# Performance work log

Hardware: AMD Instinct MI355X
Metric: run time of the kernel (lower is better)

The kernel has to match this reference:

```python
import jax, jax.numpy as jnp
import numpy as np

N = 50_000      # nodes
E = 800_000     # edges (before self-loops)
D = 128         # in_dim == out_dim
H, C = 4, 32    # GAT heads, per-head channels (out_dim // 4)
NEG_SLOPE = 0.2
LN_EPS = 1e-5


def setup_inputs() -> dict:
    key = jax.random.key(0)
    ks = jax.random.split(key, 8)
    s = 0.05
    return {
        "x": jax.random.normal(ks[0], (N, D), jnp.float32),
        "gat_W": jax.random.normal(ks[1], (D, H * C), jnp.float32) * s,
        "att_src": jax.random.normal(ks[2], (H, C), jnp.float32) * s,
        "att_dst": jax.random.normal(ks[3], (H, C), jnp.float32) * s,
        "gat_bias": jnp.zeros((H * C,), jnp.float32),
        "gcn_W": jax.random.normal(ks[4], (D, D), jnp.float32) * s,
        "gcn_bias": jnp.zeros((D,), jnp.float32),
        "gate_W": jax.random.normal(ks[5], (2 * D, 2), jnp.float32) * s,
        "gate_b": jnp.zeros((2,), jnp.float32),
        "ln_gamma": jnp.ones((D,), jnp.float32),
        "ln_beta": jnp.zeros((D,), jnp.float32),
        "edge_index": jax.random.randint(ks[6], (2, E), 0, N, jnp.int64),
    }


def reference(x, gat_W, att_src, att_dst, gat_bias, gcn_W, gcn_bias,
              gate_W, gate_b, ln_gamma, ln_beta, edge_index):
    n = x.shape[0]
    # PyG default: add self-loops for both GATConv and GCNConv
    loops = jnp.arange(n, dtype=edge_index.dtype)
    src = jnp.concatenate([edge_index[0], loops])  # message source j
    dst = jnp.concatenate([edge_index[1], loops])  # aggregation target i

    # ---------------- GATConv (heads=4, concat=True) ----------------
    h = (x @ gat_W).reshape(n, H, C)               # [N,H,C]
    a_src = jnp.einsum('nhc,hc->nh', h, att_src)   # [N,H]
    a_dst = jnp.einsum('nhc,hc->nh', h, att_dst)
    e = a_src[src] + a_dst[dst]                    # [Et,H]
    e = jnp.where(e > 0, e, NEG_SLOPE * e)         # LeakyReLU(0.2)
    e_max = jax.ops.segment_max(e, dst, num_segments=n)   # scatter-softmax, stable
    w = jnp.exp(e - e_max[dst])
    w_sum = jax.ops.segment_sum(w, dst, num_segments=n)
    alpha = w / w_sum[dst]                         # [Et,H]
    msg = alpha[:, :, None] * h[src]               # [Et,H,C]
    gat_out = jax.ops.segment_sum(msg, dst, num_segments=n).reshape(n, H * C) + gat_bias

    # ---------------- GCNConv (sym-normalized, self-loops) ----------------
    deg = jax.ops.segment_sum(jnp.ones_like(dst, dtype=x.dtype), dst, num_segments=n)
    dinv = jnp.where(deg > 0, deg ** -0.5, 0.0)
    norm = dinv[src] * dinv[dst]                   # [Et]
    g = x @ gcn_W                                  # [N,D]
    gcn_out = jax.ops.segment_sum(norm[:, None] * g[src], dst, num_segments=n) + gcn_bias

    # ---------------- gated fusion + residual + LayerNorm ----------------
    gate = jax.nn.softmax(jnp.concatenate([gat_out, gcn_out], axis=1) @ gate_W + gate_b, axis=-1)
    out = gate[:, 0:1] * gat_out + gate[:, 1:2] * gcn_out
    y = out + x
    mu = y.mean(axis=-1, keepdims=True)
    var = y.var(axis=-1, keepdims=True)
    return (y - mu) * jax.lax.rsqrt(var + LN_EPS) * ln_gamma + ln_beta
```

## Files before the change

### kernel.cpp

```cpp
#include <hip/hip_runtime.h>
#include <math.h>


typedef __attribute__((ext_vector_type(8))) short    bf16x8;
typedef __attribute__((ext_vector_type(4))) float    f32x4;
typedef __attribute__((ext_vector_type(8))) unsigned short u16x8;

__device__ __forceinline__ unsigned short f2bf(float f) {
    unsigned int u = __float_as_uint(f);
    u += 0x7fffu + ((u >> 16) & 1u);
    return (unsigned short)(u >> 16);
}
__device__ __forceinline__ float bfhi(unsigned int u) {
    return __uint_as_float(u & 0xffff0000u);
}
__device__ __forceinline__ float bflo(unsigned int u) {
    return __uint_as_float(u << 16);
}

__global__ __launch_bounds__(256) void k_prep(
    const float* __restrict__ Wg, const float* __restrict__ Wc,
    unsigned short* __restrict__ wt, int* __restrict__ counts, int n)
{
    const int t = blockIdx.x * 256 + threadIdx.x;
    const int nn = t >> 4;
    const int k0 = (t & 15) * 8;
    const float* Wsrc = (nn < 128) ? (Wg + nn) : (Wc + (nn - 128));
    u16x8 u;
    #pragma unroll
    for (int j = 0; j < 8; ++j) u[j] = f2bf(Wsrc[(size_t)(k0 + j) * 128]);
    *reinterpret_cast<u16x8*>(wt + (size_t)t * 8) = u;
    for (int i = t; i < n; i += 4096) counts[i] = 0;
}

__global__ void k_hist(const int* __restrict__ dst, int* __restrict__ counts, int E)
{
    int i = blockIdx.x * blockDim.x + threadIdx.x;
    if (i < E) atomicAdd(&counts[dst[i]], 1);
}

__global__ __launch_bounds__(256) void k_scan1(const int* __restrict__ counts,
                                               int* __restrict__ bsum, int n)
{
    __shared__ int sh[256];
    int t = threadIdx.x;
    int i = blockIdx.x * 256 + t;
    sh[t] = (i < n) ? counts[i] : 0;
    __syncthreads();
    #pragma unroll
    for (int off = 128; off >= 1; off >>= 1) {
        if (t < off) sh[t] += sh[t + off];
        __syncthreads();
    }
    if (t == 0) bsum[blockIdx.x] = sh[0];
}

__global__ __launch_bounds__(256) void k_scan2(int* __restrict__ bsum, int nb)
{
    __shared__ int sh[256];
    int t = threadIdx.x;
    int v = (t < nb) ? bsum[t] : 0;
    sh[t] = v;
    __syncthreads();
    #pragma unroll
    for (int off = 1; off < 256; off <<= 1) {
        int u = (t >= off) ? sh[t - off] : 0;
        __syncthreads();
        sh[t] += u;
        __syncthreads();
    }
    if (t < nb) bsum[t] = sh[t] - v;
}

__global__ __launch_bounds__(256) void k_scan3(
    const int* __restrict__ counts, const int* __restrict__ bsum,
    int* __restrict__ rowptr, int* __restrict__ cursor,
    float* __restrict__ dinv, int n)
{
    __shared__ int sh[256];
    int t = threadIdx.x;
    int i = blockIdx.x * 256 + t;
    int v = (i < n) ? counts[i] : 0;
    sh[t] = v;
    __syncthreads();
    #pragma unroll
    for (int off = 1; off < 256; off <<= 1) {
        int u = (t >= off) ? sh[t - off] : 0;
        __syncthreads();
        sh[t] += u;
        __syncthreads();
    }
    if (i < n) {
        int excl = bsum[blockIdx.x] + sh[t] - v;
        rowptr[i] = excl;
        cursor[i] = excl;
        dinv[i] = rsqrtf((float)(1 + v));
        if (i == n - 1) rowptr[n] = excl + v;
    }
}

__global__ __launch_bounds__(256) void k_combo(
    const float* __restrict__ x, const unsigned short* __restrict__ wt,
    const float* __restrict__ att_src, const float* __restrict__ att_dst,
    const float* __restrict__ dinv, unsigned short* __restrict__ pk,
    float* __restrict__ a_src, float* __restrict__ a_dst, int n)
{
    __shared__ unsigned short wlds[32768];
    const int t = threadIdx.x;

    char* lbase = (char*)wlds;
    #pragma unroll
    for (int i = 0; i < 16; ++i) {
        const int ch = i * 256 + t;
        const int nn = ch >> 4;
        const int off = (ch & 15) * 16;
        const int byte = (nn * 256 + off) ^ ((nn & 7) << 4);
        *reinterpret_cast<u16x8*>(lbase + byte) =
            *reinterpret_cast<const u16x8*>(wt + (size_t)ch * 8);
    }
    __syncthreads();

    const int l = t & 63;
    const int row0 = blockIdx.x * 64 + (t >> 6) * 16;
    const int arow = row0 + (l & 15);
    const bool av = arow < n;
    const float* xp = x + (size_t)arow * 128 + (l >> 4) * 8;

    bf16x8 afr[4];
    #pragma unroll
    for (int ks = 0; ks < 4; ++ks) {
        float4 u0 = av ? *reinterpret_cast<const float4*>(xp + ks * 32)
                       : make_float4(0.f, 0.f, 0.f, 0.f);
        float4 u1 = av ? *reinterpret_cast<const float4*>(xp + ks * 32 + 4)
                       : make_float4(0.f, 0.f, 0.f, 0.f);
        bf16x8 a;
        a[0] = (short)f2bf(u0.x); a[1] = (short)f2bf(u0.y);
        a[2] = (short)f2bf(u0.z); a[3] = (short)f2bf(u0.w);
        a[4] = (short)f2bf(u1.x); a[5] = (short)f2bf(u1.y);
        a[6] = (short)f2bf(u1.z); a[7] = (short)f2bf(u1.w);
        afr[ks] = a;
    }

    f32x4 acc[16];
    #pragma unroll
    for (int ni = 0; ni < 16; ++ni) acc[ni] = (f32x4){0.f, 0.f, 0.f, 0.f};

    const int bco = (l & 15) * 256 + (l >> 4) * 16;
    const int bxo = (l & 7) << 4;
    #pragma unroll
    for (int ks = 0; ks < 4; ++ks) {
        #pragma unroll
        for (int ni = 0; ni < 16; ++ni) {
            const int byte = ((ni * 16) * 256 + bco + ks * 64) ^ bxo;
            const bf16x8 b = *reinterpret_cast<const bf16x8*>(lbase + byte);
            acc[ni] = __builtin_amdgcn_mfma_f32_16x16x32_bf16(afr[ks], b, acc[ni], 0, 0, 0);
        }
    }

    float ps[4][4], pd[4][4];
    #pragma unroll
    for (int h = 0; h < 4; ++h)
        #pragma unroll
        for (int q = 0; q < 4; ++q) { ps[h][q] = 0.f; pd[h][q] = 0.f; }

    #pragma unroll
    for (int ni = 0; ni < 8; ++ni) {
        const float as = att_src[ni * 16 + (l & 15)];
        const float ad = att_dst[ni * 16 + (l & 15)];
        #pragma unroll
        for (int q = 0; q < 4; ++q) {
            ps[ni >> 1][q] += acc[ni][q] * as;
            pd[ni >> 1][q] += acc[ni][q] * ad;
        }
    }
    #pragma unroll
    for (int h = 0; h < 4; ++h) {
        #pragma unroll
        for (int q = 0; q < 4; ++q) {
            float v = ps[h][q];
            v += __shfl_xor(v, 1); v += __shfl_xor(v, 2);
            v += __shfl_xor(v, 4); v += __shfl_xor(v, 8);
            ps[h][q] = v;
            float u = pd[h][q];
            u += __shfl_xor(u, 1); u += __shfl_xor(u, 2);
            u += __shfl_xor(u, 4); u += __shfl_xor(u, 8);
            pd[h][q] = u;
        }
    }
    if ((l & 15) == 0) {
        #pragma unroll
        for (int q = 0; q < 4; ++q) {
            const int row = row0 + (l >> 4) * 4 + q;
            if (row < n) {
                *reinterpret_cast<float4*>(a_src + (size_t)row * 4) =
                    make_float4(ps[0][q], ps[1][q], ps[2][q], ps[3][q]);
                *reinterpret_cast<float4*>(a_dst + (size_t)row * 4) =
                    make_float4(pd[0][q], pd[1][q], pd[2][q], pd[3][q]);
            }
        }
    }

    const int m = l & 15;
    const int mo = m & 1;
    #pragma unroll
    for (int q = 0; q < 4; ++q) {
        const int row = row0 + (l >> 4) * 4 + q;
        if (row >= n) continue;
        const float dv = dinv[row];
        unsigned short* pr = pk + (size_t)row * 256;
        #pragma unroll
        for (int ni = 0; ni < 8; ++ni) {
            const int c = ni * 16 + m;
            pr[2 * c - mo] = f2bf(acc[ni][q]);
        }
        #pragma unroll
        for (int ni = 8; ni < 16; ++ni) {
            const int cp = (ni - 8) * 16 + m;
            pr[2 * cp + 2 - mo] = f2bf(acc[ni][q] * dv);
        }
    }
}

__global__ void k_scatter(const int* __restrict__ src, const int* __restrict__ dst,
                          int* __restrict__ cursor, int* __restrict__ esorted, int E)
{
    int i = blockIdx.x * blockDim.x + threadIdx.x;
    if (i < E) {
        int p = atomicAdd(&cursor[dst[i]], 1);
        esorted[p] = src[i];
    }
}

__global__ __launch_bounds__(256) void k_fused(
    const int* __restrict__ esorted, const int* __restrict__ rowptr,
    const uint2* __restrict__ pkv,
    const float* __restrict__ a_src, const float* __restrict__ a_dst,
    const float* __restrict__ dinv, const float* __restrict__ x,
    const float* __restrict__ gat_bias, const float* __restrict__ gcn_bias,
    const float* __restrict__ gate_W, const float* __restrict__ gate_b,
    const float* __restrict__ gamma, const float* __restrict__ beta,
    float* __restrict__ out, int n)
{
    const int lane = threadIdx.x & 63;
    const int node = blockIdx.x * 4 + (threadIdx.x >> 6);
    if (node >= n) return;

    const int head = lane >> 4;
    const float adh = a_dst[node * 4 + head];
    const int beg = rowptr[node], end = rowptr[node + 1];

    float acc0 = 0.f, acc1 = 0.f, accg0 = 0.f, accg1 = 0.f, ws = 0.f;

#define ELOAD(i) \
    const int s##i = esorted[j + i]; \
    const uint2 f##i = pkv[(size_t)s##i * 64 + lane]; \
    const float a##i = a_src[s##i * 4 + head];

#define EBODY(i) \
    { \
        float e = a##i + adh; e = e > 0.f ? e : 0.2f * e; \
        const float w = __expf(e); ws += w; \
        acc0  = fmaf(w, bflo(f##i.x), acc0); \
        acc1  = fmaf(w, bfhi(f##i.x), acc1); \
        accg0 += bflo(f##i.y); \
        accg1 += bfhi(f##i.y); \
    }

    int j = beg;
    for (; j + 8 <= end; j += 8) {
        ELOAD(0) ELOAD(1) ELOAD(2) ELOAD(3)
        ELOAD(4) ELOAD(5) ELOAD(6) ELOAD(7)
        EBODY(0) EBODY(1) EBODY(2) EBODY(3)
        EBODY(4) EBODY(5) EBODY(6) EBODY(7)
    }
    for (; j + 4 <= end; j += 4) {
        ELOAD(0) ELOAD(1) ELOAD(2) ELOAD(3)
        EBODY(0) EBODY(1) EBODY(2) EBODY(3)
    }
    for (; j < end; ++j) {
        ELOAD(0)
        EBODY(0)
    }

    {
        const uint2 f = pkv[(size_t)node * 64 + lane];
        float e = a_src[node * 4 + head] + adh;
        e = e > 0.f ? e : 0.2f * e;
        const float w = __expf(e);
        ws += w;
        acc0  = fmaf(w, bflo(f.x), acc0);
        acc1  = fmaf(w, bfhi(f.x), acc1);
        accg0 += bflo(f.y);
        accg1 += bfhi(f.y);
    }
#undef ELOAD
#undef EBODY

    const float dvd = dinv[node];
    const float2 gb2 = *reinterpret_cast<const float2*>(gat_bias + 2 * lane);
    const float2 gc2 = *reinterpret_cast<const float2*>(gcn_bias + 2 * lane);
    const float iws = 1.f / ws;
    float ga0 = acc0 * iws + gb2.x;
    float ga1 = acc1 * iws + gb2.y;
    float gc0 = accg0 * dvd + gc2.x;
    float gc1 = accg1 * dvd + gc2.y;

    const float4 gwa = *reinterpret_cast<const float4*>(gate_W + 4 * lane);
    const float4 gwb = *reinterpret_cast<const float4*>(gate_W + 256 + 4 * lane);
    float z0 = ga0 * gwa.x + ga1 * gwa.z + gc0 * gwb.x + gc1 * gwb.z;
    float z1 = ga0 * gwa.y + ga1 * gwa.w + gc0 * gwb.y + gc1 * gwb.w;
    #pragma unroll
    for (int off = 32; off >= 1; off >>= 1) {
        z0 += __shfl_xor(z0, off);
        z1 += __shfl_xor(z1, off);
    }
    z0 += gate_b[0]; z1 += gate_b[1];
    float m = fmaxf(z0, z1);
    float ez0 = __expf(z0 - m), ez1 = __expf(z1 - m);
    float inv = 1.f / (ez0 + ez1);
    float g0 = ez0 * inv, g1 = ez1 * inv;

    const size_t nbase = (size_t)node * 128;
    const float2 xv = *reinterpret_cast<const float2*>(x + nbase + 2 * lane);
    float y0 = g0 * ga0 + g1 * gc0 + xv.x;
    float y1 = g0 * ga1 + g1 * gc1 + xv.y;

    float sum = y0 + y1;
    #pragma unroll
    for (int off = 32; off >= 1; off >>= 1) sum += __shfl_xor(sum, off);
    float mu = sum * (1.f / 128.f);
    float d0v = y0 - mu, d1v = y1 - mu;
    float sq = d0v * d0v + d1v * d1v;
    #pragma unroll
    for (int off = 32; off >= 1; off >>= 1) sq += __shfl_xor(sq, off);
    float r = rsqrtf(sq * (1.f / 128.f) + 1e-5f);

    const float2 gm = *reinterpret_cast<const float2*>(gamma + 2 * lane);
    const float2 bt = *reinterpret_cast<const float2*>(beta + 2 * lane);
    float2 o;
    o.x = d0v * r * gm.x + bt.x;
    o.y = d1v * r * gm.y + bt.y;
    *reinterpret_cast<float2*>(out + nbase + 2 * lane) = o;
}

extern "C" void kernel_launch(void* const* d_in, const int* in_sizes, int n_in,
                              void* d_out, int out_size, void* d_ws, size_t ws_size,
                              hipStream_t stream)
{
    const float* x        = (const float*)d_in[0];
    const float* gat_W    = (const float*)d_in[1];
    const float* att_src  = (const float*)d_in[2];
    const float* att_dst  = (const float*)d_in[3];
    const float* gat_bias = (const float*)d_in[4];
    const float* gcn_W    = (const float*)d_in[5];
    const float* gcn_bias = (const float*)d_in[6];
    const float* gate_W   = (const float*)d_in[7];
    const float* gate_b   = (const float*)d_in[8];
    const float* ln_gamma = (const float*)d_in[9];
    const float* ln_beta  = (const float*)d_in[10];
    const int*   edge     = (const int*)d_in[11];

    const int n = in_sizes[0] / 128;
    const int E = in_sizes[11] / 2;
    const int* src = edge;
    const int* dst = edge + E;
    const int nb_chunks = (n + 255) / 256;

    char* w = (char*)d_ws;
    unsigned short* pk = (unsigned short*)w;  w += (size_t)n * 256 * 2;
    unsigned short* wt = (unsigned short*)w;  w += (size_t)256 * 128 * 2;
    float* a_src   = (float*)w;  w += (size_t)n * 4 * 4;
    float* a_dst   = (float*)w;  w += (size_t)n * 4 * 4;
    float* dinv    = (float*)w;  w += (size_t)n * 4;
    int*   counts  = (int*)w;    w += (size_t)n * 4;
    int*   bsum    = (int*)w;    w += (size_t)256 * 4;
    int*   rowptr  = (int*)w;    w += (size_t)(n + 1) * 4;
    int*   cursor  = (int*)w;    w += (size_t)n * 4;
    int*   esorted = (int*)w;    w += (size_t)E * 4;

    k_prep<<<16, 256, 0, stream>>>(gat_W, gcn_W, wt, counts, n);
    k_hist<<<(E + 255) / 256, 256, 0, stream>>>(dst, counts, E);
    k_scan1<<<nb_chunks, 256, 0, stream>>>(counts, bsum, n);
    k_scan2<<<1, 256, 0, stream>>>(bsum, nb_chunks);
    k_scan3<<<nb_chunks, 256, 0, stream>>>(counts, bsum, rowptr, cursor, dinv, n);
    k_combo<<<(n + 63) / 64, 256, 0, stream>>>(x, wt, att_src, att_dst, dinv,
                                               pk, a_src, a_dst, n);
    k_scatter<<<(E + 255) / 256, 256, 0, stream>>>(src, dst, cursor, esorted, E);
    k_fused<<<(n + 3) / 4, 256, 0, stream>>>(esorted, rowptr, (const uint2*)pk,
                                             a_src, a_dst, dinv, x, gat_bias, gcn_bias,
                                             gate_W, gate_b, ln_gamma, ln_beta,
                                             (float*)d_out, n);
}
```

Baseline: 278.5 us.

## Merge preprocessing kernels, single-block scan, split GEMM halves alongside scatter

Folds the weight conversion and the degree histogram into one launch and replaces the three-kernel prefix scan with a single 1024-thread block scan. The edge scatter now runs in the same launch as the projection GEMM, which is split into GAT and GCN column halves per block to halve LDS and accumulator use. Together these cut kernel launches and let scatter atomics overlap the MFMA work. The single-block scan serializes about 50 elements per thread, and the aggregation loop drops its 8-wide unroll, which may reduce memory-level parallelism.

```diff
diff --git a/kernel.cpp b/kernel.cpp
--- a/kernel.cpp
+++ b/kernel.cpp
@@ -18,110 +18,104 @@
     return __uint_as_float(u << 16);
 }
 
-__global__ __launch_bounds__(256) void k_prep(
+__global__ __launch_bounds__(256) void k_prep_hist(
     const float* __restrict__ Wg, const float* __restrict__ Wc,
-    unsigned short* __restrict__ wt, int* __restrict__ counts, int n)
-{
-    const int t = blockIdx.x * 256 + threadIdx.x;
-    const int nn = t >> 4;
-    const int k0 = (t & 15) * 8;
-    const float* Wsrc = (nn < 128) ? (Wg + nn) : (Wc + (nn - 128));
-    u16x8 u;
-    #pragma unroll
-    for (int j = 0; j < 8; ++j) u[j] = f2bf(Wsrc[(size_t)(k0 + j) * 128]);
-    *reinterpret_cast<u16x8*>(wt + (size_t)t * 8) = u;
-    for (int i = t; i < n; i += 4096) counts[i] = 0;
-}
-
-__global__ void k_hist(const int* __restrict__ dst, int* __restrict__ counts, int E)
-{
-    int i = blockIdx.x * blockDim.x + threadIdx.x;
-    if (i < E) atomicAdd(&counts[dst[i]], 1);
-}
-
-__global__ __launch_bounds__(256) void k_scan1(const int* __restrict__ counts,
-                                               int* __restrict__ bsum, int n)
-{
-    __shared__ int sh[256];
-    int t = threadIdx.x;
-    int i = blockIdx.x * 256 + t;
-    sh[t] = (i < n) ? counts[i] : 0;
+    unsigned short* __restrict__ wt, const int* __restrict__ dst,
+    int* __restrict__ counts, int E)
+{
+    const int t = threadIdx.x;
+    if (blockIdx.x < 16) {
+        const int g = blockIdx.x * 256 + t;
+        const int nn = g >> 4;
+        const int k0 = (g & 15) * 8;
+        const float* Wsrc = (nn < 128) ? (Wg + nn) : (Wc + (nn - 128));
+        u16x8 u;
+        #pragma unroll
+        for (int j = 0; j < 8; ++j) u[j] = f2bf(Wsrc[(size_t)(k0 + j) * 128]);
+        *reinterpret_cast<u16x8*>(wt + (size_t)g * 8) = u;
+        return;
+    }
+    int i = (blockIdx.x - 16) * 256 + t;
+    const int stride = (gridDim.x - 16) * 256;
+    for (; i < E; i += stride) atomicAdd(&counts[dst[i]], 1);
+}
+
+__global__ __launch_bounds__(1024) void k_scan(
+    const int* __restrict__ counts, int* __restrict__ rowptr,
+    int* __restrict__ cursor, float* __restrict__ dinv, int n)
+{
+    __shared__ int sh[1024];
+    const int t = threadIdx.x;
+    const int CH = (n + 1023) >> 10;
+    const int i0 = t * CH;
+    int s = 0;
+    for (int k = 0; k < CH; ++k) {
+        const int i = i0 + k;
+        if (i < n) s += counts[i];
+    }
+    sh[t] = s;
     __syncthreads();
-    #pragma unroll
-    for (int off = 128; off >= 1; off >>= 1) {
-        if (t < off) sh[t] += sh[t + off];
-        __syncthreads();
-    }
-    if (t == 0) bsum[blockIdx.x] = sh[0];
-}
-
-__global__ __launch_bounds__(256) void k_scan2(int* __restrict__ bsum, int nb)
-{
-    __shared__ int sh[256];
-    int t = threadIdx.x;
-    int v = (t < nb) ? bsum[t] : 0;
-    sh[t] = v;
-    __syncthreads();
-    #pragma unroll
-    for (int off = 1; off < 256; off <<= 1) {
-        int u = (t >= off) ? sh[t - off] : 0;
+    for (int off = 1; off < 1024; off <<= 1) {
+        const int u = (t >= off) ? sh[t - off] : 0;
         __syncthreads();
         sh[t] += u;
         __syncthreads();
     }
-    if (t < nb) bsum[t] = sh[t] - v;
-}
-
-__global__ __launch_bounds__(256) void k_scan3(
-    const int* __restrict__ counts, const int* __restrict__ bsum,
-    int* __restrict__ rowptr, int* __restrict__ cursor,
-    float* __restrict__ dinv, int n)
-{
-    __shared__ int sh[256];
-    int t = threadIdx.x;
-    int i = blockIdx.x * 256 + t;
-    int v = (i < n) ? counts[i] : 0;
-    sh[t] = v;
-    __syncthreads();
-    #pragma unroll
-    for (int off = 1; off < 256; off <<= 1) {
-        int u = (t >= off) ? sh[t - off] : 0;
-        __syncthreads();
-        sh[t] += u;
-        __syncthreads();
-    }
-    if (i < n) {
-        int excl = bsum[blockIdx.x] + sh[t] - v;
-        rowptr[i] = excl;
-        cursor[i] = excl;
-        dinv[i] = rsqrtf((float)(1 + v));
-        if (i == n - 1) rowptr[n] = excl + v;
-    }
-}
-
-__global__ __launch_bounds__(256) void k_combo(
+    int run = sh[t] - s;
+    for (int k = 0; k < CH; ++k) {
+        const int i = i0 + k;
+        if (i < n) {
+            const int v = counts[i];
+            rowptr[i] = run;
+            cursor[i] = run;
+            dinv[i] = rsqrtf((float)(1 + v));
+            run += v;
+        }
+    }
+    if (t == 1023) rowptr[n] = sh[1023];
+}
+
+__global__ __launch_bounds__(256) void k_combo_scatter(
     const float* __restrict__ x, const unsigned short* __restrict__ wt,
     const float* __restrict__ att_src, const float* __restrict__ att_dst,
-    const float* __restrict__ dinv, unsigned short* __restrict__ pk,
-    float* __restrict__ a_src, float* __restrict__ a_dst, int n)
-{
-    __shared__ unsigned short wlds[32768];
+    const float* __restrict__ dinv, const int* __restrict__ src,
+    const int* __restrict__ dst, int* __restrict__ cursor,
+    int* __restrict__ esorted, unsigned short* __restrict__ pk,
+    float* __restrict__ a_src, float* __restrict__ a_dst,
+    int n, int E, int scatBlocks)
+{
+    __shared__ unsigned short wlds[16384];
     const int t = threadIdx.x;
 
+    if (blockIdx.x < scatBlocks) {
+        int i = blockIdx.x * 256 + t;
+        const int stride = scatBlocks * 256;
+        for (; i < E; i += stride) {
+            const int p = atomicAdd(&cursor[dst[i]], 1);
+            esorted[p] = src[i];
+        }
+        return;
+    }
+
+    const int gb = blockIdx.x - scatBlocks;
+    const int half = gb & 1;
+    const int gtile = gb >> 1;
+
     char* lbase = (char*)wlds;
     #pragma unroll
-    for (int i = 0; i < 16; ++i) {
-        const int ch = i * 256 + t;
+    for (int i2 = 0; i2 < 8; ++i2) {
+        const int ch = i2 * 256 + t;
         const int nn = ch >> 4;
         const int off = (ch & 15) * 16;
         const int byte = (nn * 256 + off) ^ ((nn & 7) << 4);
         *reinterpret_cast<u16x8*>(lbase + byte) =
-            *reinterpret_cast<const u16x8*>(wt + (size_t)ch * 8);
+            *reinterpret_cast<const u16x8*>(
+                wt + (size_t)(half * 128 + nn) * 128 + (ch & 15) * 8);
     }
     __syncthreads();
 
     const int l = t & 63;
-    const int row0 = blockIdx.x * 64 + (t >> 6) * 16;
+    const int row0 = gtile * 64 + (t >> 6) * 16;
     const int arow = row0 + (l & 15);
     const bool av = arow < n;
     const float* xp = x + (size_t)arow * 128 + (l >> 4) * 8;
@@ -141,93 +135,91 @@
         afr[ks] = a;
     }
 
-    f32x4 acc[16];
-    #pragma unroll
-    for (int ni = 0; ni < 16; ++ni) acc[ni] = (f32x4){0.f, 0.f, 0.f, 0.f};
+    f32x4 acc[8];
+    #pragma unroll
+    for (int ni = 0; ni < 8; ++ni) acc[ni] = (f32x4){0.f, 0.f, 0.f, 0.f};
 
     const int bco = (l & 15) * 256 + (l >> 4) * 16;
     const int bxo = (l & 7) << 4;
     #pragma unroll
     for (int ks = 0; ks < 4; ++ks) {
         #pragma unroll
-        for (int ni = 0; ni < 16; ++ni) {
+        for (int ni = 0; ni < 8; ++ni) {
             const int byte = ((ni * 16) * 256 + bco + ks * 64) ^ bxo;
             const bf16x8 b = *reinterpret_cast<const bf16x8*>(lbase + byte);
             acc[ni] = __builtin_amdgcn_mfma_f32_16x16x32_bf16(afr[ks], b, acc[ni], 0, 0, 0);
         }
     }
 
-    float ps[4][4], pd[4][4];
-    #pragma unroll
-    for (int h = 0; h < 4; ++h)
-        #pragma unroll
-        for (int q = 0; q < 4; ++q) { ps[h][q] = 0.f; pd[h][q] = 0.f; }
-
-    #pragma unroll
-    for (int ni = 0; ni < 8; ++ni) {
-        const float as = att_src[ni * 16 + (l & 15)];
-        const float ad = att_dst[ni * 16 + (l & 15)];
-        #pragma unroll
-        for (int q = 0; q < 4; ++q) {
-            ps[ni >> 1][q] += acc[ni][q] * as;
-            pd[ni >> 1][q] += acc[ni][q] * ad;
-        }
-    }
-    #pragma unroll
-    for (int h = 0; h < 4; ++h) {
-        #pragma unroll
-        for (int q = 0; q < 4; ++q) {
-            float v = ps[h][q];
-            v += __shfl_xor(v, 1); v += __shfl_xor(v, 2);
-            v += __shfl_xor(v, 4); v += __shfl_xor(v, 8);
-            ps[h][q] = v;
-            float u = pd[h][q];
-            u += __shfl_xor(u, 1); u += __shfl_xor(u, 2);
-            u += __shfl_xor(u, 4); u += __shfl_xor(u, 8);
-            pd[h][q] = u;
-        }
-    }
-    if ((l & 15) == 0) {
+    const int m = l & 15;
+    const int mo = m & 1;
+
+    if (half == 0) {
+        float ps[4][4], pd[4][4];
+        #pragma unroll
+        for (int h = 0; h < 4; ++h)
+            #pragma unroll
+            for (int q = 0; q < 4; ++q) { ps[h][q] = 0.f; pd[h][q] = 0.f; }
+        #pragma unroll
+        for (int ni = 0; ni < 8; ++ni) {
+            const float as = att_src[ni * 16 + m];
+            const float ad = att_dst[ni * 16 + m];
+            #pragma unroll
+            for (int q = 0; q < 4; ++q) {
+                ps[ni >> 1][q] += acc[ni][q] * as;
+                pd[ni >> 1][q] += acc[ni][q] * ad;
+            }
+        }
+        #pragma unroll
+        for (int h = 0; h < 4; ++h) {
+            #pragma unroll
+            for (int q = 0; q < 4; ++q) {
+                float v = ps[h][q];
+                v += __shfl_xor(v, 1); v += __shfl_xor(v, 2);
+                v += __shfl_xor(v, 4); v += __shfl_xor(v, 8);
+                ps[h][q] = v;
+                float u = pd[h][q];
+                u += __shfl_xor(u, 1); u += __shfl_xor(u, 2);
+                u += __shfl_xor(u, 4); u += __shfl_xor(u, 8);
+                pd[h][q] = u;
+            }
+        }
+        if (m == 0) {
+            #pragma unroll
+            for (int q = 0; q < 4; ++q) {
+                const int row = row0 + (l >> 4) * 4 + q;
+                if (row < n) {
+                    *reinterpret_cast<float4*>(a_src + (size_t)row * 4) =
+                        make_float4(ps[0][q], ps[1][q], ps[2][q], ps[3][q]);
+                    *reinterpret_cast<float4*>(a_dst + (size_t)row * 4) =
+                        make_float4(pd[0][q], pd[1][q], pd[2][q], pd[3][q]);
+                }
+            }
+        }
         #pragma unroll
         for (int q = 0; q < 4; ++q) {
             const int row = row0 + (l >> 4) * 4 + q;
-            if (row < n) {
-                *reinterpret_cast<float4*>(a_src + (size_t)row * 4) =
-                    make_float4(ps[0][q], ps[1][q], ps[2][q], ps[3][q]);
-                *reinterpret_cast<float4*>(a_dst + (size_t)row * 4) =
-                    make_float4(pd[0][q], pd[1][q], pd[2][q], pd[3][q]);
-            }
-        }
-    }
-
-    const int m = l & 15;
-    const int mo = m & 1;
-    #pragma unroll
-    for (int q = 0; q < 4; ++q) {
-        const int row = row0 + (l >> 4) * 4 + q;
-        if (row >= n) continue;
-        const float dv = dinv[row];
-        unsigned short* pr = pk + (size_t)row * 256;
-        #pragma unroll
-        for (int ni = 0; ni < 8; ++ni) {
-            const int c = ni * 16 + m;
-            pr[2 * c - mo] = f2bf(acc[ni][q]);
-        }
-        #pragma unroll
-        for (int ni = 8; ni < 16; ++ni) {
-            const int cp = (ni - 8) * 16 + m;
-            pr[2 * cp + 2 - mo] = f2bf(acc[ni][q] * dv);
-        }
-    }
-}
-
-__global__ void k_scatter(const int* __restrict__ src, const int* __restrict__ dst,
-                          int* __restrict__ cursor, int* __restrict__ esorted, int E)
-{
-    int i = blockIdx.x * blockDim.x + threadIdx.x;
-    if (i < E) {
-        int p = atomicAdd(&cursor[dst[i]], 1);
-        esorted[p] = src[i];
+            if (row >= n) continue;
+            unsigned short* pr = pk + (size_t)row * 256;
+            #pragma unroll
+            for (int ni = 0; ni < 8; ++ni) {
+                const int c = ni * 16 + m;
+                pr[2 * c - mo] = f2bf(acc[ni][q]);
+            }
+        }
+    } else {
+        #pragma unroll
+        for (int q = 0; q < 4; ++q) {
+            const int row = row0 + (l >> 4) * 4 + q;
+            if (row >= n) continue;
+            const float dv = dinv[row];
+            unsigned short* pr = pk + (size_t)row * 256;
+            #pragma unroll
+            for (int ni = 0; ni < 8; ++ni) {
+                const int cp = ni * 16 + m;
+                pr[2 * cp + 2 - mo] = f2bf(acc[ni][q] * dv);
+            }
+        }
     }
 }
 
@@ -267,12 +259,6 @@
     }
 
     int j = beg;
-    for (; j + 8 <= end; j += 8) {
-        ELOAD(0) ELOAD(1) ELOAD(2) ELOAD(3)
-        ELOAD(4) ELOAD(5) ELOAD(6) ELOAD(7)
-        EBODY(0) EBODY(1) EBODY(2) EBODY(3)
-        EBODY(4) EBODY(5) EBODY(6) EBODY(7)
-    }
     for (; j + 4 <= end; j += 4) {
         ELOAD(0) ELOAD(1) ELOAD(2) ELOAD(3)
         EBODY(0) EBODY(1) EBODY(2) EBODY(3)
@@ -364,7 +350,6 @@
     const int E = in_sizes[11] / 2;
     const int* src = edge;
     const int* dst = edge + E;
-    const int nb_chunks = (n + 255) / 256;
 
     char* w = (char*)d_ws;
     unsigned short* pk = (unsigned short*)w;  w += (size_t)n * 256 * 2;
@@ -373,19 +358,21 @@
     float* a_dst   = (float*)w;  w += (size_t)n * 4 * 4;
     float* dinv    = (float*)w;  w += (size_t)n * 4;
     int*   counts  = (int*)w;    w += (size_t)n * 4;
-    int*   bsum    = (int*)w;    w += (size_t)256 * 4;
     int*   rowptr  = (int*)w;    w += (size_t)(n + 1) * 4;
     int*   cursor  = (int*)w;    w += (size_t)n * 4;
     int*   esorted = (int*)w;    w += (size_t)E * 4;
 
-    k_prep<<<16, 256, 0, stream>>>(gat_W, gcn_W, wt, counts, n);
-    k_hist<<<(E + 255) / 256, 256, 0, stream>>>(dst, counts, E);
-    k_scan1<<<nb_chunks, 256, 0, stream>>>(counts, bsum, n);
-    k_scan2<<<1, 256, 0, stream>>>(bsum, nb_chunks);
-    k_scan3<<<nb_chunks, 256, 0, stream>>>(counts, bsum, rowptr, cursor, dinv, n);
-    k_combo<<<(n + 63) / 64, 256, 0, stream>>>(x, wt, att_src, att_dst, dinv,
-                                               pk, a_src, a_dst, n);
-    k_scatter<<<(E + 255) / 256, 256, 0, stream>>>(src, dst, cursor, esorted, E);
+    hipMemsetAsync(counts, 0, (size_t)n * 4, stream);
+
+    const int histBlocks = 1024;
+    const int scatBlocks = 1024;
+    const int gemmBlocks = 2 * ((n + 63) / 64);
+
+    k_prep_hist<<<16 + histBlocks, 256, 0, stream>>>(gat_W, gcn_W, wt, dst, counts, E);
+    k_scan<<<1, 1024, 0, stream>>>(counts, rowptr, cursor, dinv, n);
+    k_combo_scatter<<<scatBlocks + gemmBlocks, 256, 0, stream>>>(
+        x, wt, att_src, att_dst, dinv, src, dst, cursor, esorted,
+        pk, a_src, a_dst, n, E, scatBlocks);
     k_fused<<<(n + 3) / 4, 256, 0, stream>>>(esorted, rowptr, (const uint2*)pk,
                                              a_src, a_dst, dinv, x, gat_bias, gcn_bias,
                                              gate_W, gate_b, ln_gamma, ln_beta,
```

Measured after the change: 420.1 us. 50.9% more time.
